# Performance work log

Hardware: AMD Instinct MI355X
Metric: run time of the kernel (lower is better)

The kernel has to match this reference:

```python
import jax, jax.numpy as jnp
import numpy as np
from jax import lax

B, N = 4, 32768          # clouds, points per cloud (offsets are equal-sized)
CIN, COUT, S = 128, 256, 2048  # in_channels, out_channels, num_samples
EPS = 1e-5               # BatchNorm eps


def fps(xyz, npoint=S):
    """Farthest point sampling over xyz [N,3]; deterministic start index 0.
    Mirrors the torch loop: record current farthest, update min-distance, argmax."""
    n = xyz.shape[0]

    def step(carry, _):
        distance, farthest = carry
        centroid = xyz[farthest]                       # [3]
        dist = jnp.sum((xyz - centroid) ** 2, axis=1)  # [N]
        distance = jnp.minimum(distance, dist)
        new_farthest = jnp.argmax(distance).astype(jnp.int32)
        return (distance, new_farthest), farthest

    init = (jnp.full((n,), 1e10, dtype=xyz.dtype), jnp.int32(0))
    _, centroids = lax.scan(step, init, None, length=npoint)
    return centroids  # [npoint] int32


def setup_inputs():
    key = jax.random.key(0)
    k1, k2, k3 = jax.random.split(key, 3)
    coord = jax.random.normal(k1, (B * N, 3), dtype=jnp.float32)
    feat = jax.random.normal(k2, (B * N, CIN), dtype=jnp.float32)
    offset = (jnp.arange(1, B + 1, dtype=jnp.int32)) * N  # cumulative counts
    W = jax.random.normal(k3, (COUT, CIN), dtype=jnp.float32) / np.sqrt(CIN)
    gamma = jnp.ones((COUT,), dtype=jnp.float32)
    beta = jnp.zeros((COUT,), dtype=jnp.float32)
    return {"coord": coord, "feat": feat, "offset": offset,
            "W": W, "gamma": gamma, "beta": beta}


def reference(coord, feat, offset, W, gamma, beta):
    # fc -> PointBatchNorm (training-mode batch stats over B*N rows) -> ReLU
    x = feat @ W.T                                  # [B*N, COUT]
    mean = jnp.mean(x, axis=0)
    var = jnp.mean((x - mean) ** 2, axis=0)         # biased var, as torch BN
    x = (x - mean) * lax.rsqrt(var + EPS) * gamma + beta
    x = jax.nn.relu(x)

    coord_b = coord.reshape(B, N, 3)
    feat_b = x.reshape(B, N, COUT)
    idx = jax.vmap(fps)(coord_b)                    # [B, S] int32

    new_coords = jnp.take_along_axis(coord_b, idx[..., None], axis=1).reshape(B * S, 3)
    new_feats = jnp.take_along_axis(feat_b, idx[..., None], axis=1).reshape(B * S, COUT)
    new_offsets = jnp.arange(1, B + 1, dtype=jnp.int32) * S
    return new_coords, new_feats, new_offsets
```

## Files before the change

### kernel.cpp

```cpp
#include <hip/hip_runtime.h>

#define NB 4
#define NPT 32768
#define QPT 8192
#define CIN 128
#define COUT 256
#define NS 2048
#define THR 512
#define PPT 16

#define WS_G 0
#define WS_FSUM 16384
#define WS_SLOT 16512
#define WS_GSCALE 16768
#define WS_GBIAS 17024
#define WS_IDX 17280

#define OUT_COORD 0
#define OUT_FEAT 24576
#define OUT_OFFS 2121728

__global__ __launch_bounds__(THR) void fused1(
    const float* __restrict__ coord, const float* __restrict__ feat,
    float* __restrict__ wsf, int* __restrict__ wsi,
    unsigned long long* __restrict__ slots)
{
  __shared__ float2 lxy[QPT];
  __shared__ float lz[QPT];
  __shared__ unsigned long long s_key[2];
  __shared__ float s_fs[4][128];

  const int bid = blockIdx.x;
  const int t = threadIdx.x;
  const bool is_fps = (bid < 32) && ((bid & 7) < 4);

  if (is_fps) {
    const int cl = bid & 3;
    const int h = bid >> 3;
    const int gbase = h * QPT;
    const float* xyz = coord + (size_t)cl * NPT * 3;
    int* idx_out = wsi + cl * NS;
    unsigned long long* slot = slots + cl * 32;

    float dv[PPT];
#pragma unroll
    for (int j = 0; j < PPT; ++j) {
      const int l = j * THR + t;
      const int p = gbase + l;
      lxy[l] = make_float2(xyz[p * 3 + 0], xyz[p * 3 + 1]);
      lz[l] = xyz[p * 3 + 2];
      dv[j] = 1e10f;
    }
    if (t == 0) {
      if (h == 0) idx_out[0] = 0;
      s_key[0] = s_key[1] = 0ull;
    }
    float cx = xyz[0], cy = xyz[1], cz = xyz[2];
    __syncthreads();

    const int lane = t & 63;
    for (int it = 1; it < NS; ++it) {
      const int par = it & 1;
      const unsigned long long utag = (unsigned long long)it;
      float bd = -1.f;
      int bj = 0;
#pragma unroll
      for (int j = 0; j < PPT; ++j) {
        const int l = j * THR + t;
        const float2 xy = lxy[l];
        const float zz = lz[l];
        float dx = xy.x - cx, dy = xy.y - cy, dz = zz - cz;
        float sx = dx * dx, sy = dy * dy, sz = dz * dz;
        asm volatile("" : "+v"(sx), "+v"(sy), "+v"(sz));
        float nd = fminf(dv[j], (sx + sy) + sz);
        dv[j] = nd;
        if (nd > bd) { bd = nd; bj = j; }
      }
      const int gidx = gbase + bj * THR + t;
      const unsigned long long tkey =
          (utag << 48) |
          ((unsigned long long)(unsigned)__float_as_int(bd) << 15) |
          (unsigned)(32767 - gidx);
      unsigned long long wkey = tkey;
#pragma unroll
      for (int o = 32; o > 0; o >>= 1) {
        unsigned long long ok = __shfl_xor(wkey, o, 64);
        wkey = ok > wkey ? ok : wkey;
      }
      if (lane == 0) atomicMax(&s_key[par], wkey);
      __syncthreads();
      const unsigned long long skey = s_key[par];
      if (tkey == skey)
        __hip_atomic_store(&slot[par * 4 + h], skey,
                           __ATOMIC_RELAXED, __HIP_MEMORY_SCOPE_AGENT);
      unsigned long long v = 0;
      for (;;) {
        if (lane < 4)
          v = __hip_atomic_load(&slot[par * 4 + lane],
                                __ATOMIC_RELAXED, __HIP_MEMORY_SCOPE_AGENT);
        const bool ok = (lane >= 4) || ((v >> 48) == utag);
        if (__all((int)ok)) break;
        __builtin_amdgcn_s_sleep(1);
      }
      unsigned long long o1 = __shfl_xor(v, 1, 64);
      v = o1 > v ? o1 : v;
      unsigned long long o2 = __shfl_xor(v, 2, 64);
      v = o2 > v ? o2 : v;
      v = __shfl(v, 0, 64);
      const int widx = 32767 - (int)(v & 0x7fff);
      if (h == 0 && t == 0) idx_out[it] = widx;
      cx = xyz[widx * 3 + 0];
      cy = xyz[widx * 3 + 1];
      cz = xyz[widx * 3 + 2];
    }
  } else {
    const int g = (bid < 32) ? ((bid >> 3) * 4 + (bid & 7) - 4) : (bid - 16);
    if (g < 128) {
      const float* fr = feat + (size_t)g * 1024 * CIN;
      const int ti = (t & 31) * 4;
      const int tj = (t >> 5) * 8;
      float acc[4][8];
#pragma unroll
      for (int a = 0; a < 4; ++a)
#pragma unroll
        for (int b2 = 0; b2 < 8; ++b2) acc[a][b2] = 0.f;
#pragma unroll 4
      for (int r = 0; r < 1024; ++r) {
        const float* rowp = fr + r * CIN;
        float4 a4 = *(const float4*)(rowp + ti);
        float4 b4 = *(const float4*)(rowp + tj);
        float4 b5 = *(const float4*)(rowp + tj + 4);
        float av[4] = {a4.x, a4.y, a4.z, a4.w};
        float bv[8] = {b4.x, b4.y, b4.z, b4.w, b5.x, b5.y, b5.z, b5.w};
#pragma unroll
        for (int a = 0; a < 4; ++a)
#pragma unroll
          for (int b2 = 0; b2 < 8; ++b2) acc[a][b2] += av[a] * bv[b2];
      }
      float* G = wsf + WS_G;
#pragma unroll
      for (int a = 0; a < 4; ++a)
#pragma unroll
        for (int b2 = 0; b2 < 8; ++b2)
          atomicAdd(&G[(ti + a) * CIN + (tj + b2)], acc[a][b2]);
    } else {
      const int fb = g - 128;
      const size_t base = (size_t)fb * 16384;
      const int c = t & 127, rg = t >> 7;
      float s = 0.f;
      for (int r = rg; r < 16384; r += 4)
        s += feat[(base + r) * CIN + c];
      s_fs[rg][c] = s;
      __syncthreads();
      if (t < 128) {
        float v = s_fs[0][t] + s_fs[1][t] + s_fs[2][t] + s_fs[3][t];
        atomicAdd(&wsf[WS_FSUM + t], v);
      }
    }
  }
}

__global__ __launch_bounds__(128) void finalize_k(
    const float* __restrict__ W, const float* __restrict__ gamma,
    const float* __restrict__ beta, float* __restrict__ wsf)
{
  const int c = blockIdx.x, i = threadIdx.x;
  const float* G = wsf + WS_G;
  const float* fsum = wsf + WS_FSUM;
  const float* Gi = G + i * CIN;
  const float* Wc = W + c * CIN;
  float td = 0.f;
#pragma unroll 8
  for (int j = 0; j < CIN; j += 4) {
    float4 g4 = *(const float4*)(Gi + j);
    float4 w4 = *(const float4*)(Wc + j);
    td += g4.x * w4.x + g4.y * w4.y + g4.z * w4.z + g4.w * w4.w;
  }
  const float wci = Wc[i];
  float q = wci * td;
  float m = fsum[i] * wci;
#pragma unroll
  for (int o = 32; o > 0; o >>= 1) {
    q += __shfl_xor(q, o, 64);
    m += __shfl_xor(m, o, 64);
  }
  __shared__ float sq[2], sm[2];
  if ((i & 63) == 0) { sq[i >> 6] = q; sm[i >> 6] = m; }
  __syncthreads();
  if (i == 0) {
    const float inv_m = 1.f / 131072.f;
    float mean = (sm[0] + sm[1]) * inv_m;
    float e2 = (sq[0] + sq[1]) * inv_m;
    float var = e2 - mean * mean;
    float rstd = rsqrtf(var + 1e-5f);
    float gs = gamma[c] * rstd;
    wsf[WS_GSCALE + c] = gs;
    wsf[WS_GBIAS + c] = beta[c] - mean * gs;
  }
}

__global__ __launch_bounds__(256) void gather_k(
    const float* __restrict__ coord, const float* __restrict__ feat,
    const float* __restrict__ W, const float* __restrict__ wsf,
    const int* __restrict__ wsi, float* __restrict__ out)
{
  const int p = blockIdx.x, t = threadIdx.x;
  const int b = p >> 11;
  const int idx = wsi[p];
  const size_t row = (size_t)b * NPT + idx;
  __shared__ float lf[CIN];
  if (t < CIN) lf[t] = feat[row * CIN + t];
  __syncthreads();
  const float* Wc = W + t * CIN;
  float acc = 0.f;
#pragma unroll 8
  for (int k = 0; k < CIN; k += 4) {
    float4 w4 = *(const float4*)(Wc + k);
    acc += lf[k] * w4.x + lf[k + 1] * w4.y + lf[k + 2] * w4.z + lf[k + 3] * w4.w;
  }
  float y = fmaxf(fmaf(acc, wsf[WS_GSCALE + t], wsf[WS_GBIAS + t]), 0.f);
  out[OUT_FEAT + (size_t)p * COUT + t] = y;
  if (t < 3) out[OUT_COORD + p * 3 + t] = coord[row * 3 + t];
  if (p == 0 && t < 4) out[OUT_OFFS + t] = (float)((t + 1) * NS);
}

extern "C" void kernel_launch(void* const* d_in, const int* in_sizes, int n_in,
                              void* d_out, int out_size, void* d_ws, size_t ws_size,
                              hipStream_t stream)
{
  const float* coord = (const float*)d_in[0];
  const float* feat  = (const float*)d_in[1];
  const float* W     = (const float*)d_in[3];
  const float* gamma = (const float*)d_in[4];
  const float* beta  = (const float*)d_in[5];
  float* wsf = (float*)d_ws;
  int* wsi = (int*)(wsf + WS_IDX);
  unsigned long long* slots = (unsigned long long*)(wsf + WS_SLOT);
  float* out = (float*)d_out;

  hipMemsetAsync(d_ws, 0, (WS_SLOT + 256) * sizeof(float), stream);

  fused1<<<152, THR, 0, stream>>>(coord, feat, wsf, wsi, slots);
  finalize_k<<<COUT, 128, 0, stream>>>(W, gamma, beta, wsf);
  gather_k<<<NB * NS, 256, 0, stream>>>(coord, feat, W, wsf, wsi, out);
}
```

Before: 4.421 ms.

## Pad FPS cross-block sync slots and poll with sc0 loads, with an atomic fallback

The per-cloud cross-block exchange slots are now spaced 256 bytes apart so that each slot sits in its own cache line, and the workspace offsets and memset size grow to match. Each winning thread writes its key with a raw sc0 global store plus the atomic store. Pollers first use sc0 global loads, which may be cheaper than agent-scope atomics, and switch a lane to the atomic load for the rest of the kernel once it has failed FASTN times. The aim is lower latency in the 2047 serial inter-block handshakes of farthest point sampling. The risk is that a stale cached value on the fast path adds retries before the fallback applies.

```diff
diff --git a/kernel.cpp b/kernel.cpp
--- a/kernel.cpp
+++ b/kernel.cpp
@@ -8,13 +8,14 @@
 #define NS 2048
 #define THR 512
 #define PPT 16
+#define FASTN 10
 
 #define WS_G 0
 #define WS_FSUM 16384
 #define WS_SLOT 16512
-#define WS_GSCALE 16768
-#define WS_GBIAS 17024
-#define WS_IDX 17280
+#define WS_GSCALE 18560
+#define WS_GBIAS 18816
+#define WS_IDX 19072
 
 #define OUT_COORD 0
 #define OUT_FEAT 24576
@@ -40,7 +41,7 @@
     const int gbase = h * QPT;
     const float* xyz = coord + (size_t)cl * NPT * 3;
     int* idx_out = wsi + cl * NS;
-    unsigned long long* slot = slots + cl * 32;
+    unsigned long long* slot = slots + (size_t)cl * 256;
 
     float dv[PPT];
 #pragma unroll
@@ -59,6 +60,8 @@
     __syncthreads();
 
     const int lane = t & 63;
+    unsigned fastmask = 0xFu;
+
     for (int it = 1; it < NS; ++it) {
       const int par = it & 1;
       const unsigned long long utag = (unsigned long long)it;
@@ -90,17 +93,34 @@
       if (lane == 0) atomicMax(&s_key[par], wkey);
       __syncthreads();
       const unsigned long long skey = s_key[par];
-      if (tkey == skey)
-        __hip_atomic_store(&slot[par * 4 + h], skey,
+      if (tkey == skey) {
+        unsigned long long* myslot = &slot[(par * 4 + h) * 32];
+        asm volatile("global_store_dwordx2 %0, %1, off sc0"
+                     :: "v"(myslot), "v"(skey) : "memory");
+        __hip_atomic_store(myslot, skey,
                            __ATOMIC_RELAXED, __HIP_MEMORY_SCOPE_AGENT);
+      }
       unsigned long long v = 0;
-      for (;;) {
-        if (lane < 4)
-          v = __hip_atomic_load(&slot[par * 4 + lane],
-                                __ATOMIC_RELAXED, __HIP_MEMORY_SCOPE_AGENT);
-        const bool ok = (lane >= 4) || ((v >> 48) == utag);
-        if (__all((int)ok)) break;
-        __builtin_amdgcn_s_sleep(1);
+      if (lane < 4) {
+        const unsigned long long* addr = &slot[(par * 4 + lane) * 32];
+        bool fast = (fastmask >> lane) & 1u;
+        int tries = 0;
+        for (;;) {
+          if (fast) {
+            asm volatile("global_load_dwordx2 %0, %1, off sc0\n\t"
+                         "s_waitcnt vmcnt(0)"
+                         : "=v"(v) : "v"(addr) : "memory");
+          } else {
+            v = __hip_atomic_load(addr, __ATOMIC_RELAXED,
+                                  __HIP_MEMORY_SCOPE_AGENT);
+          }
+          if ((v >> 48) == utag) break;
+          if (fast && ++tries >= FASTN) {
+            fast = false;
+            fastmask &= ~(1u << lane);
+          }
+          __builtin_amdgcn_s_sleep(1);
+        }
       }
       unsigned long long o1 = __shfl_xor(v, 1, 64);
       v = o1 > v ? o1 : v;
@@ -238,7 +258,7 @@
   unsigned long long* slots = (unsigned long long*)(wsf + WS_SLOT);
   float* out = (float*)d_out;
 
-  hipMemsetAsync(d_ws, 0, (WS_SLOT + 256) * sizeof(float), stream);
+  hipMemsetAsync(d_ws, 0, (WS_SLOT + 2048) * sizeof(float), stream);
 
   fused1<<<152, THR, 0, stream>>>(coord, feat, wsf, wsi, slots);
   finalize_k<<<COUT, 128, 0, stream>>>(W, gamma, beta, wsf);
```

Measured after the change: 5.025 ms. 1.14x slower.

## Replace intra-block barrier with per-wave global slots in FPS argmax sync

Applied to the files above, without the earlier changes.

Each wavefront now publishes its own argmax key to a per-cluster global slot array of 32 entries (4 blocks x 8 waves). Wave 0 of each block polls all 32 slots, reduces them, and broadcasts the winner through LDS. The other waves spin on that LDS word, which removes the shared atomicMax and the __syncthreads from every FPS iteration. The trade-off is more global slots to poll, LDS spin loops in the non-leader waves, and a larger workspace and memset.

```diff
diff --git a/kernel.cpp b/kernel.cpp
--- a/kernel.cpp
+++ b/kernel.cpp
@@ -12,9 +12,9 @@
 #define WS_G 0
 #define WS_FSUM 16384
 #define WS_SLOT 16512
-#define WS_GSCALE 16768
-#define WS_GBIAS 17024
-#define WS_IDX 17280
+#define WS_GSCALE 17536
+#define WS_GBIAS 17792
+#define WS_IDX 18048
 
 #define OUT_COORD 0
 #define OUT_FEAT 24576
@@ -27,7 +27,7 @@
 {
   __shared__ float2 lxy[QPT];
   __shared__ float lz[QPT];
-  __shared__ unsigned long long s_key[2];
+  __shared__ unsigned long long s_res[2];
   __shared__ float s_fs[4][128];
 
   const int bid = blockIdx.x;
@@ -40,7 +40,7 @@
     const int gbase = h * QPT;
     const float* xyz = coord + (size_t)cl * NPT * 3;
     int* idx_out = wsi + cl * NS;
-    unsigned long long* slot = slots + cl * 32;
+    unsigned long long* slotc = slots + (size_t)cl * 128;
 
     float dv[PPT];
 #pragma unroll
@@ -53,15 +53,19 @@
     }
     if (t == 0) {
       if (h == 0) idx_out[0] = 0;
-      s_key[0] = s_key[1] = 0ull;
+      s_res[0] = s_res[1] = 0ull;
     }
     float cx = xyz[0], cy = xyz[1], cz = xyz[2];
     __syncthreads();
 
     const int lane = t & 63;
+    const int wid = t >> 6;
+    const int wslot = h * 8 + wid;
+
     for (int it = 1; it < NS; ++it) {
       const int par = it & 1;
       const unsigned long long utag = (unsigned long long)it;
+      unsigned long long* slotp = slotc + par * 32;
       float bd = -1.f;
       int bj = 0;
 #pragma unroll
@@ -77,38 +81,45 @@
         if (nd > bd) { bd = nd; bj = j; }
       }
       const int gidx = gbase + bj * THR + t;
-      const unsigned long long tkey =
+      unsigned long long wkey =
           (utag << 48) |
           ((unsigned long long)(unsigned)__float_as_int(bd) << 15) |
           (unsigned)(32767 - gidx);
-      unsigned long long wkey = tkey;
 #pragma unroll
       for (int o = 32; o > 0; o >>= 1) {
         unsigned long long ok = __shfl_xor(wkey, o, 64);
         wkey = ok > wkey ? ok : wkey;
       }
-      if (lane == 0) atomicMax(&s_key[par], wkey);
-      __syncthreads();
-      const unsigned long long skey = s_key[par];
-      if (tkey == skey)
-        __hip_atomic_store(&slot[par * 4 + h], skey,
+      if (lane == 0)
+        __hip_atomic_store(&slotp[wslot], wkey,
                            __ATOMIC_RELAXED, __HIP_MEMORY_SCOPE_AGENT);
-      unsigned long long v = 0;
-      for (;;) {
-        if (lane < 4)
-          v = __hip_atomic_load(&slot[par * 4 + lane],
+      unsigned long long res;
+      if (wid == 0) {
+        unsigned long long v;
+        for (;;) {
+          v = __hip_atomic_load(&slotp[lane & 31],
                                 __ATOMIC_RELAXED, __HIP_MEMORY_SCOPE_AGENT);
-        const bool ok = (lane >= 4) || ((v >> 48) == utag);
-        if (__all((int)ok)) break;
-        __builtin_amdgcn_s_sleep(1);
-      }
-      unsigned long long o1 = __shfl_xor(v, 1, 64);
-      v = o1 > v ? o1 : v;
-      unsigned long long o2 = __shfl_xor(v, 2, 64);
-      v = o2 > v ? o2 : v;
-      v = __shfl(v, 0, 64);
-      const int widx = 32767 - (int)(v & 0x7fff);
-      if (h == 0 && t == 0) idx_out[it] = widx;
+          if (__all((int)((v >> 48) == utag))) break;
+          __builtin_amdgcn_s_sleep(1);
+        }
+#pragma unroll
+        for (int o = 16; o > 0; o >>= 1) {
+          unsigned long long ov = __shfl_xor(v, o, 64);
+          v = ov > v ? ov : v;
+        }
+        if (lane == 0) {
+          __hip_atomic_store(&s_res[par], v,
+                             __ATOMIC_RELAXED, __HIP_MEMORY_SCOPE_WORKGROUP);
+          if (h == 0) idx_out[it] = 32767 - (int)(v & 0x7fff);
+        }
+        res = __shfl(v, 0, 64);
+      } else {
+        do {
+          res = __hip_atomic_load(&s_res[par],
+                                  __ATOMIC_RELAXED, __HIP_MEMORY_SCOPE_WORKGROUP);
+        } while ((res >> 48) != utag);
+      }
+      const int widx = 32767 - (int)(res & 0x7fff);
       cx = xyz[widx * 3 + 0];
       cy = xyz[widx * 3 + 1];
       cz = xyz[widx * 3 + 2];
@@ -238,7 +249,7 @@
   unsigned long long* slots = (unsigned long long*)(wsf + WS_SLOT);
   float* out = (float*)d_out;
 
-  hipMemsetAsync(d_ws, 0, (WS_SLOT + 256) * sizeof(float), stream);
+  hipMemsetAsync(d_ws, 0, (WS_SLOT + 1024) * sizeof(float), stream);
 
   fused1<<<152, THR, 0, stream>>>(coord, feat, wsf, wsi, slots);
   finalize_k<<<COUT, 128, 0, stream>>>(W, gamma, beta, wsf);
```

Measured after the change: 7.020 ms. 58.8% more time.

## Publish FPS winner coordinates through sync slots and poll with one wave

Applied to the files above, without the earlier changes.

Each FPS block that holds the winning point now writes its coordinates, packed into two tagged 64-bit words, next to the argmax key in the cross-block slots. Readers therefore get the next centroid directly from the sync exchange instead of issuing a dependent global load of xyz[widx] after the barrier. Only wave 0 polls the global slots. It then broadcasts the result through LDS, where the other waves spin. The aim is to shorten the serial per-iteration critical path, at the cost of more polled words per exchange and LDS spinning by seven waves.

```diff
diff --git a/kernel.cpp b/kernel.cpp
--- a/kernel.cpp
+++ b/kernel.cpp
@@ -28,6 +28,7 @@
   __shared__ float2 lxy[QPT];
   __shared__ float lz[QPT];
   __shared__ unsigned long long s_key[2];
+  __shared__ unsigned long long s_res[2][2];
   __shared__ float s_fs[4][128];
 
   const int bid = blockIdx.x;
@@ -40,7 +41,7 @@
     const int gbase = h * QPT;
     const float* xyz = coord + (size_t)cl * NPT * 3;
     int* idx_out = wsi + cl * NS;
-    unsigned long long* slot = slots + cl * 32;
+    unsigned long long* slotc = slots + (size_t)cl * 32;
 
     float dv[PPT];
 #pragma unroll
@@ -54,11 +55,15 @@
     if (t == 0) {
       if (h == 0) idx_out[0] = 0;
       s_key[0] = s_key[1] = 0ull;
+      s_res[0][0] = s_res[0][1] = 0ull;
+      s_res[1][0] = s_res[1][1] = 0ull;
     }
     float cx = xyz[0], cy = xyz[1], cz = xyz[2];
     __syncthreads();
 
     const int lane = t & 63;
+    const int wid = t >> 6;
+
     for (int it = 1; it < NS; ++it) {
       const int par = it & 1;
       const unsigned long long utag = (unsigned long long)it;
@@ -90,28 +95,68 @@
       if (lane == 0) atomicMax(&s_key[par], wkey);
       __syncthreads();
       const unsigned long long skey = s_key[par];
-      if (tkey == skey)
-        __hip_atomic_store(&slot[par * 4 + h], skey,
+      if (tkey == skey) {
+        const int l = bj * THR + t;
+        const unsigned cxb = __float_as_uint(lxy[l].x);
+        const unsigned cyb = __float_as_uint(lxy[l].y);
+        const unsigned czb = __float_as_uint(lz[l]);
+        const unsigned long long w1 =
+            (utag << 48) | ((unsigned long long)cxb << 16) | (cyb >> 16);
+        const unsigned long long w2 =
+            (utag << 48) | ((unsigned long long)(cyb & 0xFFFFu) << 32) | czb;
+        unsigned long long* myslot = &slotc[par * 16 + h * 4];
+        __hip_atomic_store(&myslot[0], skey,
                            __ATOMIC_RELAXED, __HIP_MEMORY_SCOPE_AGENT);
-      unsigned long long v = 0;
-      for (;;) {
-        if (lane < 4)
-          v = __hip_atomic_load(&slot[par * 4 + lane],
-                                __ATOMIC_RELAXED, __HIP_MEMORY_SCOPE_AGENT);
-        const bool ok = (lane >= 4) || ((v >> 48) == utag);
-        if (__all((int)ok)) break;
-        __builtin_amdgcn_s_sleep(1);
-      }
-      unsigned long long o1 = __shfl_xor(v, 1, 64);
-      v = o1 > v ? o1 : v;
-      unsigned long long o2 = __shfl_xor(v, 2, 64);
-      v = o2 > v ? o2 : v;
-      v = __shfl(v, 0, 64);
-      const int widx = 32767 - (int)(v & 0x7fff);
-      if (h == 0 && t == 0) idx_out[it] = widx;
-      cx = xyz[widx * 3 + 0];
-      cy = xyz[widx * 3 + 1];
-      cz = xyz[widx * 3 + 2];
+        __hip_atomic_store(&myslot[1], w1,
+                           __ATOMIC_RELAXED, __HIP_MEMORY_SCOPE_AGENT);
+        __hip_atomic_store(&myslot[2], w2,
+                           __ATOMIC_RELAXED, __HIP_MEMORY_SCOPE_AGENT);
+      }
+      unsigned long long res1, res2;
+      if (wid == 0) {
+        unsigned long long v = 0;
+        unsigned long long* base = &slotc[par * 16];
+        for (;;) {
+          if (lane < 16)
+            v = __hip_atomic_load(&base[lane],
+                                  __ATOMIC_RELAXED, __HIP_MEMORY_SCOPE_AGENT);
+          const bool ok = (lane >= 16) || ((lane & 3) == 3) ||
+                          ((v >> 48) == utag);
+          if (__all((int)ok)) break;
+          __builtin_amdgcn_s_sleep(1);
+        }
+        const unsigned long long k0 = __shfl(v, 0, 64);
+        const unsigned long long k1 = __shfl(v, 4, 64);
+        const unsigned long long k2 = __shfl(v, 8, 64);
+        const unsigned long long k3 = __shfl(v, 12, 64);
+        unsigned long long kb = k0; int wb = 0;
+        if (k1 > kb) { kb = k1; wb = 1; }
+        if (k2 > kb) { kb = k2; wb = 2; }
+        if (k3 > kb) { kb = k3; wb = 3; }
+        res1 = __shfl(v, wb * 4 + 1, 64);
+        res2 = __shfl(v, wb * 4 + 2, 64);
+        if (lane == 0) {
+          __hip_atomic_store(&s_res[par][0], res1,
+                             __ATOMIC_RELAXED, __HIP_MEMORY_SCOPE_WORKGROUP);
+          __hip_atomic_store(&s_res[par][1], res2,
+                             __ATOMIC_RELAXED, __HIP_MEMORY_SCOPE_WORKGROUP);
+          if (h == 0) idx_out[it] = 32767 - (int)(kb & 0x7fff);
+        }
+      } else {
+        do {
+          res1 = __hip_atomic_load(&s_res[par][0],
+                                   __ATOMIC_RELAXED, __HIP_MEMORY_SCOPE_WORKGROUP);
+          res2 = __hip_atomic_load(&s_res[par][1],
+                                   __ATOMIC_RELAXED, __HIP_MEMORY_SCOPE_WORKGROUP);
+        } while (((res1 >> 48) != utag) || ((res2 >> 48) != utag));
+      }
+      const unsigned cxb = (unsigned)((res1 >> 16) & 0xFFFFFFFFull);
+      const unsigned cyb = (unsigned)(((res1 & 0xFFFFull) << 16) |
+                                      ((res2 >> 32) & 0xFFFFull));
+      const unsigned czb = (unsigned)(res2 & 0xFFFFFFFFull);
+      cx = __uint_as_float(cxb);
+      cy = __uint_as_float(cyb);
+      cz = __uint_as_float(czb);
     }
   } else {
     const int g = (bid < 32) ? ((bid >> 3) * 4 + (bid & 7) - 4) : (bid - 16);
```

New measurement: 5.568 ms. 25.9% more time.
